# Kernel optimization log

Hardware: AMD Instinct MI355X
Metric: run time of the kernel (lower is better)

## Reference

```python
import jax, jax.numpy as jnp
import numpy as np

B, N, M, D = 4, 2048, 4096, 1
C, K = 4, 32
POINTS_PER_UNIT = 20


def setup_inputs() -> dict:
    key = jax.random.key(0)
    k1, k2, k3 = jax.random.split(key, 3)
    xz = jax.random.uniform(k1, (M, D), dtype=jnp.float32) * 4.0 - 2.0  # grid locations
    x = jax.random.uniform(k2, (B, N, D), dtype=jnp.float32) * 4.0 - 2.0  # target locations
    z = jax.random.normal(k3, (B, C, M, K), dtype=jnp.float32)
    log_scale = jnp.array([np.log(2.0 / POINTS_PER_UNIT)], dtype=jnp.float32)
    return {"xz": xz, "x": x, "z": z, "log_scale": log_scale}


def reference(xz, x, z, log_scale):
    # pairwise squared distances between grid xz [M,D] and targets x [B,N,D] -> [B,M,N]
    d2 = jnp.sum((xz[None, :, None, :] - x[:, None, :, :]) ** 2, axis=-1)
    # RBF weights (note: divided by exp(log_scale), matching original code)
    w = jnp.exp(-0.5 * d2 / jnp.exp(log_scale[0]))  # [B,M,N]
    # weights^T @ z with channel broadcast: [B,C,N,K]
    zt = jnp.einsum('bmn,bcmk->bcnk', w, z)
    # outer product z @ z^T: [B,C,N,N] positive semi-definite
    out = jnp.einsum('bcnk,bcmk->bcnm', zt, zt)
    return (xz, out)
```

## Files before the change

### kernel.cpp

```cpp
#include <hip/hip_runtime.h>
#include <hip/hip_bf16.h>

#define B_   4
#define N_   2048
#define M_   4096
#define C_   4
#define K_   32
#define CK_  128
#define M32_ (M_ / 32)

typedef float f32x4 __attribute__((ext_vector_type(4)));
typedef short s16x8 __attribute__((ext_vector_type(8)));

__device__ __forceinline__ short f2bf(float f) {
    union { __hip_bfloat16 h; short s; } u;
    u.h = __float2bfloat16(f);
    return u.s;
}
__device__ __forceinline__ float bf2f(unsigned short u) {
    return __uint_as_float((unsigned)u << 16);
}

__global__ __launch_bounds__(256) void z2frag_kernel(
    const float* __restrict__ z, unsigned short* __restrict__ zf)
{
    const unsigned u = blockIdx.x * 256 + threadIdx.x;
    const int s   = u & 63;
    const int lg  = s >> 4, l15 = s & 15;
    const int m32 = (u >> 6) & (M32_ - 1);
    const int g   = (u >> 13) & 7;
    const int b   = u >> 16;
    const int c   = g >> 1;
    const int k   = (g & 1) * 16 + l15;
    const int m0  = m32 * 32 + lg * 8;

    const float* src = &z[(((size_t)(b * C_ + c)) * M_ + m0) * K_ + k];
    s16x8 pk;
    #pragma unroll
    for (int e = 0; e < 8; ++e) pk[e] = f2bf(src[(size_t)e * K_]);
    *(s16x8*)&zf[(size_t)u * 8] = pk;
}

template <int MS>
__global__ __launch_bounds__(512, 4) void zt_mfma_kernel(
    const float* __restrict__ xz, const float* __restrict__ x,
    const unsigned short* __restrict__ zf, const float* __restrict__ ls,
    unsigned short* __restrict__ ztp)
{
    constexpr int MCH = M_ / MS;
    constexpr int L   = MCH / 32;
    __shared__ __align__(16) float xz_s[MCH];

    const int tid  = threadIdx.x;
    const int lane = tid & 63;
    const int w    = tid >> 6;
    const int wq   = w >> 1;
    const int wc   = w & 1;
    const int l15  = lane & 15;
    const int lg   = lane >> 4;
    const int ms   = blockIdx.x;
    const int nblk = blockIdx.y * 128;
    const int b    = blockIdx.z;

    const float coef = -0.5f * __expf(-ls[0]);

    float xv[2];
    #pragma unroll
    for (int fa = 0; fa < 2; ++fa)
        xv[fa] = x[b * N_ + nblk + wq * 32 + fa * 16 + l15];

    const int mstart = ms * MCH;
    for (int i = tid; i < MCH; i += 512) xz_s[i] = xz[mstart + i];
    __syncthreads();

    f32x4 acc[2][4];
    #pragma unroll
    for (int i = 0; i < 2; ++i)
        #pragma unroll
        for (int j = 0; j < 4; ++j) acc[i][j] = (f32x4)0.0f;

    const unsigned short* fbase =
        &zf[(((size_t)(b * 8 + wc * 4)) * M32_ + mstart / 32) * 512 + lane * 8];

    s16x8 nb[4];
    #pragma unroll
    for (int fc = 0; fc < 4; ++fc)
        nb[fc] = *(const s16x8*)&fbase[(size_t)fc * M32_ * 512];

    #pragma unroll 4
    for (int ms32 = 0; ms32 < L; ++ms32) {
        s16x8 cb[4];
        #pragma unroll
        for (int fc = 0; fc < 4; ++fc) cb[fc] = nb[fc];
        if (ms32 + 1 < L) {
            #pragma unroll
            for (int fc = 0; fc < 4; ++fc)
                nb[fc] = *(const s16x8*)&fbase[((size_t)fc * M32_ + ms32 + 1) * 512];
        }
        const float* xzp = &xz_s[ms32 * 32 + lg * 8];
        const f32x4 t0 = *reinterpret_cast<const f32x4*>(xzp);
        const f32x4 t1 = *reinterpret_cast<const f32x4*>(xzp + 4);
        const float tt[8] = {t0.x, t0.y, t0.z, t0.w, t1.x, t1.y, t1.z, t1.w};
        s16x8 af[2];
        #pragma unroll
        for (int fa = 0; fa < 2; ++fa) {
            #pragma unroll
            for (int j = 0; j < 8; ++j) {
                const float d = tt[j] - xv[fa];
                af[fa][j] = f2bf(__expf(coef * d * d));
            }
        }
        #pragma unroll
        for (int fa = 0; fa < 2; ++fa)
            #pragma unroll
            for (int fc = 0; fc < 4; ++fc)
                acc[fa][fc] = __builtin_amdgcn_mfma_f32_16x16x32_bf16(
                    af[fa], cb[fc], acc[fa][fc], 0, 0, 0);
    }

    unsigned short* dst = ztp + (size_t)ms * (B_ * C_ * N_ * K_);
    #pragma unroll
    for (int fc = 0; fc < 4; ++fc) {
        const int ck = wc * 64 + fc * 16 + l15;
        const int c  = ck >> 5, k = ck & 31;
        #pragma unroll
        for (int fa = 0; fa < 2; ++fa) {
            const int n0 = nblk + wq * 32 + fa * 16 + lg * 4;
            #pragma unroll
            for (int r = 0; r < 4; ++r)
                dst[(((size_t)b * C_ + c) * N_ + n0 + r) * K_ + k] =
                    (unsigned short)f2bf(acc[fa][fc][r]);
        }
    }
}

template <int MS>
__global__ __launch_bounds__(256) void zt_reduce_copy_kernel(
    const unsigned short* __restrict__ ztp, unsigned short* __restrict__ ztb,
    const float* __restrict__ xz, float* __restrict__ out)
{
    if (blockIdx.x >= 1024) {
        const int t = (blockIdx.x - 1024) * 256 + threadIdx.x;
        *(float4*)&out[t * 4] = *(const float4*)&xz[t * 4];
        return;
    }
    const size_t t      = (size_t)blockIdx.x * 256 + threadIdx.x;
    const size_t stride = (size_t)(B_ * C_ * N_ * K_);
    float s0 = 0.f, s1 = 0.f, s2 = 0.f, s3 = 0.f;
    #pragma unroll
    for (int p = 0; p < MS; ++p) {
        const ushort4 v = *(const ushort4*)&ztp[(size_t)p * stride + t * 4];
        s0 += bf2f(v.x); s1 += bf2f(v.y); s2 += bf2f(v.z); s3 += bf2f(v.w);
    }
    ushort4 pk;
    pk.x = (unsigned short)f2bf(s0); pk.y = (unsigned short)f2bf(s1);
    pk.z = (unsigned short)f2bf(s2); pk.w = (unsigned short)f2bf(s3);
    *(ushort4*)&ztb[t * 4] = pk;
}

#define TB 128
__global__ __launch_bounds__(256, 4) void out_mfma_kernel(
    const unsigned short* __restrict__ ztb, float* __restrict__ out)
{
    __shared__ __align__(16) float t_s[64][132];

    const int tid  = threadIdx.x;
    const int lane = tid & 63;
    const int wave = tid >> 6;
    const int wn   = wave >> 1;
    const int wm   = wave & 1;
    const int l15  = lane & 15;
    const int lg   = lane >> 4;
    const int mblk = blockIdx.x * TB;
    const int nblk = blockIdx.y * TB;
    const int bc   = blockIdx.z;

    const unsigned short* base = ztb + (size_t)bc * (N_ * K_);

    s16x8 afr[4], bfr[4];
    #pragma unroll
    for (int f = 0; f < 4; ++f) {
        const int n = nblk + wn * 64 + f * 16 + l15;
        afr[f] = *reinterpret_cast<const s16x8*>(&base[(size_t)n * K_ + lg * 8]);
        const int m = mblk + wm * 64 + f * 16 + l15;
        bfr[f] = *reinterpret_cast<const s16x8*>(&base[(size_t)m * K_ + lg * 8]);
    }

    f32x4 acc[4][4];
    #pragma unroll
    for (int i = 0; i < 4; ++i)
        #pragma unroll
        for (int j = 0; j < 4; ++j) acc[i][j] = (f32x4)0.0f;

    #pragma unroll
    for (int fa = 0; fa < 4; ++fa)
        #pragma unroll
        for (int fm = 0; fm < 4; ++fm)
            acc[fa][fm] = __builtin_amdgcn_mfma_f32_16x16x32_bf16(
                afr[fa], bfr[fm], acc[fa][fm], 0, 0, 0);

    float* ob = out + (size_t)bc * N_ * N_;

    #pragma unroll
    for (int p = 0; p < 2; ++p) {
        if (p) __syncthreads();
        if (wn == p) {
            #pragma unroll
            for (int fa = 0; fa < 4; ++fa) {
                const int row0 = fa * 16 + lg * 4;
                #pragma unroll
                for (int fm = 0; fm < 4; ++fm) {
                    const int mcol = wm * 64 + fm * 16 + l15;
                    #pragma unroll
                    for (int r = 0; r < 4; ++r)
                        t_s[row0 + r][mcol] = acc[fa][fm][r];
                }
            }
        }
        __syncthreads();
        #pragma unroll
        for (int it = 0; it < 8; ++it) {
            const int e   = tid + it * 256;
            const int row = e >> 5;
            const int c4  = e & 31;
            const f32x4 v = *reinterpret_cast<const f32x4*>(&t_s[row][c4 * 4]);
            *(f32x4*)&ob[(size_t)(nblk + p * 64 + row) * N_ + mblk + c4 * 4] = v;
        }
    }
}

extern "C" void kernel_launch(void* const* d_in, const int* in_sizes, int n_in,
                              void* d_out, int out_size, void* d_ws, size_t ws_size,
                              hipStream_t stream)
{
    const float* xz = (const float*)d_in[0];
    const float* x  = (const float*)d_in[1];
    const float* z  = (const float*)d_in[2];
    const float* ls = (const float*)d_in[3];
    float* out = (float*)d_out;

    (void)in_sizes; (void)n_in; (void)out_size;

    const size_t ztf = (size_t)B_ * C_ * N_ * K_;
    unsigned short* ztb = (unsigned short*)d_ws;
    unsigned short* zf  = ztb + ztf;
    unsigned short* ztp = zf + (size_t)B_ * CK_ * M_;

    z2frag_kernel<<<dim3((unsigned)(B_ * 8 * M32_ * 64 / 256)), dim3(256), 0, stream>>>(z, zf);

    const size_t base_b = ztf * 2 + (size_t)B_ * CK_ * M_ * 2;
    if (ws_size >= base_b + (size_t)8 * ztf * 2) {
        zt_mfma_kernel<8><<<dim3(8, N_ / 128, B_), dim3(512), 0, stream>>>(xz, x, zf, ls, ztp);
        zt_reduce_copy_kernel<8><<<dim3(1028), dim3(256), 0, stream>>>(ztp, ztb, xz, out);
    } else if (ws_size >= base_b + (size_t)4 * ztf * 2) {
        zt_mfma_kernel<4><<<dim3(4, N_ / 128, B_), dim3(512), 0, stream>>>(xz, x, zf, ls, ztp);
        zt_reduce_copy_kernel<4><<<dim3(1028), dim3(256), 0, stream>>>(ztp, ztb, xz, out);
    } else {
        zt_mfma_kernel<2><<<dim3(2, N_ / 128, B_), dim3(512), 0, stream>>>(xz, x, zf, ls, ztp);
        zt_reduce_copy_kernel<2><<<dim3(1028), dim3(256), 0, stream>>>(ztp, ztb, xz, out);
    }

    out_mfma_kernel<<<dim3(N_ / TB, N_ / TB, B_ * C_), dim3(256), 0, stream>>>(ztb, out + M_);
}
```

Measured before the change: 82.56 us.

## Fuse all stages into one persistent kernel with atomic grid barriers

Merges the z fragment conversion, the partial zt MFMA, the split-M reduction and the output outer-product GEMM into a single 512-block persistent kernel. Stages are separated by software grid barriers built on atomic counters, which are reset by a memset before the launch. The aim is to remove the launch overhead and tail gaps of four separate kernels. In exchange the output stage now runs on only 512 blocks looping over 8 tiles each. The barriers also risk deadlock if all 512 blocks are not co-resident, and the larger shared-memory footprint may lower occupancy.

Result: slower. 273.2 us (+230.9%).

```diff
diff --git a/kernel.cpp b/kernel.cpp
--- a/kernel.cpp
+++ b/kernel.cpp
@@ -7,7 +7,10 @@
 #define C_   4
 #define K_   32
 #define CK_  128
-#define M32_ (M_ / 32)
+#define M32_ 128
+#define NBLK 512
+#define THR  512
+#define MS   8
 
 typedef float f32x4 __attribute__((ext_vector_type(4)));
 typedef short s16x8 __attribute__((ext_vector_type(8)));
@@ -21,193 +24,187 @@
     return __uint_as_float((unsigned)u << 16);
 }
 
-__global__ __launch_bounds__(256) void z2frag_kernel(
-    const float* __restrict__ z, unsigned short* __restrict__ zf)
+__device__ __forceinline__ void gridbar(unsigned* c) {
+    __syncthreads();
+    if (threadIdx.x == 0) {
+        __hip_atomic_fetch_add(c, 1u, __ATOMIC_RELEASE, __HIP_MEMORY_SCOPE_AGENT);
+        while (__hip_atomic_load(c, __ATOMIC_ACQUIRE, __HIP_MEMORY_SCOPE_AGENT) < (unsigned)NBLK)
+            __builtin_amdgcn_s_sleep(2);
+    }
+    __syncthreads();
+}
+
+__global__ __launch_bounds__(THR, 4) void fused_kernel(
+    const float* __restrict__ xz, const float* __restrict__ x,
+    const float* __restrict__ z,  const float* __restrict__ ls,
+    float* __restrict__ out, unsigned short* __restrict__ ztb,
+    unsigned short* __restrict__ zf, unsigned short* __restrict__ ztp,
+    unsigned* __restrict__ cnt)
 {
-    const unsigned u = blockIdx.x * 256 + threadIdx.x;
-    const int s   = u & 63;
-    const int lg  = s >> 4, l15 = s & 15;
-    const int m32 = (u >> 6) & (M32_ - 1);
-    const int g   = (u >> 13) & 7;
-    const int b   = u >> 16;
-    const int c   = g >> 1;
-    const int k   = (g & 1) * 16 + l15;
-    const int m0  = m32 * 32 + lg * 8;
-
-    const float* src = &z[(((size_t)(b * C_ + c)) * M_ + m0) * K_ + k];
-    s16x8 pk;
-    #pragma unroll
-    for (int e = 0; e < 8; ++e) pk[e] = f2bf(src[(size_t)e * K_]);
-    *(s16x8*)&zf[(size_t)u * 8] = pk;
-}
-
-template <int MS>
-__global__ __launch_bounds__(512, 4) void zt_mfma_kernel(
-    const float* __restrict__ xz, const float* __restrict__ x,
-    const unsigned short* __restrict__ zf, const float* __restrict__ ls,
-    unsigned short* __restrict__ ztp)
-{
-    constexpr int MCH = M_ / MS;
-    constexpr int L   = MCH / 32;
-    __shared__ __align__(16) float xz_s[MCH];
+    __shared__ __align__(16) float xz_s[M_ / MS];
+    __shared__ __align__(16) float t_s[128][132];
 
     const int tid  = threadIdx.x;
+    const int bid  = blockIdx.x;
+    const int gid  = bid * THR + tid;
     const int lane = tid & 63;
-    const int w    = tid >> 6;
-    const int wq   = w >> 1;
-    const int wc   = w & 1;
     const int l15  = lane & 15;
     const int lg   = lane >> 4;
-    const int ms   = blockIdx.x;
-    const int nblk = blockIdx.y * 128;
-    const int b    = blockIdx.z;
-
-    const float coef = -0.5f * __expf(-ls[0]);
-
-    float xv[2];
-    #pragma unroll
-    for (int fa = 0; fa < 2; ++fa)
-        xv[fa] = x[b * N_ + nblk + wq * 32 + fa * 16 + l15];
-
-    const int mstart = ms * MCH;
-    for (int i = tid; i < MCH; i += 512) xz_s[i] = xz[mstart + i];
-    __syncthreads();
-
-    f32x4 acc[2][4];
-    #pragma unroll
-    for (int i = 0; i < 2; ++i)
-        #pragma unroll
-        for (int j = 0; j < 4; ++j) acc[i][j] = (f32x4)0.0f;
-
-    const unsigned short* fbase =
-        &zf[(((size_t)(b * 8 + wc * 4)) * M32_ + mstart / 32) * 512 + lane * 8];
-
-    s16x8 nb[4];
-    #pragma unroll
-    for (int fc = 0; fc < 4; ++fc)
-        nb[fc] = *(const s16x8*)&fbase[(size_t)fc * M32_ * 512];
-
-    #pragma unroll 4
-    for (int ms32 = 0; ms32 < L; ++ms32) {
-        s16x8 cb[4];
-        #pragma unroll
-        for (int fc = 0; fc < 4; ++fc) cb[fc] = nb[fc];
-        if (ms32 + 1 < L) {
-            #pragma unroll
-            for (int fc = 0; fc < 4; ++fc)
-                nb[fc] = *(const s16x8*)&fbase[((size_t)fc * M32_ + ms32 + 1) * 512];
-        }
-        const float* xzp = &xz_s[ms32 * 32 + lg * 8];
-        const f32x4 t0 = *reinterpret_cast<const f32x4*>(xzp);
-        const f32x4 t1 = *reinterpret_cast<const f32x4*>(xzp + 4);
-        const float tt[8] = {t0.x, t0.y, t0.z, t0.w, t1.x, t1.y, t1.z, t1.w};
-        s16x8 af[2];
-        #pragma unroll
-        for (int fa = 0; fa < 2; ++fa) {
-            #pragma unroll
-            for (int j = 0; j < 8; ++j) {
-                const float d = tt[j] - xv[fa];
-                af[fa][j] = f2bf(__expf(coef * d * d));
-            }
-        }
+    const int w    = tid >> 6;
+
+    {
+        const unsigned u = (unsigned)gid;
+        const int s   = u & 63;
+        const int m32 = (u >> 6) & (M32_ - 1);
+        const int g   = (u >> 13) & 7;
+        const int b   = u >> 16;
+        const int k   = (g & 1) * 16 + (s & 15);
+        const int m0  = m32 * 32 + (s >> 4) * 8;
+        const float* src = &z[(((size_t)(b * C_ + (g >> 1))) * M_ + m0) * K_ + k];
+        s16x8 pk;
+        #pragma unroll
+        for (int e = 0; e < 8; ++e) pk[e] = f2bf(src[(size_t)e * K_]);
+        *(s16x8*)&zf[(size_t)u * 8] = pk;
+        if (gid < 1024) *(f32x4*)&out[gid * 4] = *(const f32x4*)&xz[gid * 4];
+    }
+    gridbar(cnt + 0);
+
+    {
+        constexpr int MCH = M_ / MS;
+        constexpr int L   = MCH / 32;
+        const int ms   = bid & 7;
+        const int nblk = ((bid >> 3) & 15) * 128;
+        const int b    = bid >> 7;
+        const int wq   = w >> 1;
+        const int wc   = w & 1;
+
+        const float coef = -0.5f * __expf(-ls[0]);
+        float xv[2];
         #pragma unroll
         for (int fa = 0; fa < 2; ++fa)
-            #pragma unroll
-            for (int fc = 0; fc < 4; ++fc)
-                acc[fa][fc] = __builtin_amdgcn_mfma_f32_16x16x32_bf16(
-                    af[fa], cb[fc], acc[fa][fc], 0, 0, 0);
-    }
-
-    unsigned short* dst = ztp + (size_t)ms * (B_ * C_ * N_ * K_);
-    #pragma unroll
-    for (int fc = 0; fc < 4; ++fc) {
-        const int ck = wc * 64 + fc * 16 + l15;
-        const int c  = ck >> 5, k = ck & 31;
-        #pragma unroll
-        for (int fa = 0; fa < 2; ++fa) {
-            const int n0 = nblk + wq * 32 + fa * 16 + lg * 4;
-            #pragma unroll
-            for (int r = 0; r < 4; ++r)
-                dst[(((size_t)b * C_ + c) * N_ + n0 + r) * K_ + k] =
-                    (unsigned short)f2bf(acc[fa][fc][r]);
-        }
-    }
-}
-
-template <int MS>
-__global__ __launch_bounds__(256) void zt_reduce_copy_kernel(
-    const unsigned short* __restrict__ ztp, unsigned short* __restrict__ ztb,
-    const float* __restrict__ xz, float* __restrict__ out)
-{
-    if (blockIdx.x >= 1024) {
-        const int t = (blockIdx.x - 1024) * 256 + threadIdx.x;
-        *(float4*)&out[t * 4] = *(const float4*)&xz[t * 4];
-        return;
-    }
-    const size_t t      = (size_t)blockIdx.x * 256 + threadIdx.x;
-    const size_t stride = (size_t)(B_ * C_ * N_ * K_);
-    float s0 = 0.f, s1 = 0.f, s2 = 0.f, s3 = 0.f;
-    #pragma unroll
-    for (int p = 0; p < MS; ++p) {
-        const ushort4 v = *(const ushort4*)&ztp[(size_t)p * stride + t * 4];
-        s0 += bf2f(v.x); s1 += bf2f(v.y); s2 += bf2f(v.z); s3 += bf2f(v.w);
-    }
-    ushort4 pk;
-    pk.x = (unsigned short)f2bf(s0); pk.y = (unsigned short)f2bf(s1);
-    pk.z = (unsigned short)f2bf(s2); pk.w = (unsigned short)f2bf(s3);
-    *(ushort4*)&ztb[t * 4] = pk;
-}
-
-#define TB 128
-__global__ __launch_bounds__(256, 4) void out_mfma_kernel(
-    const unsigned short* __restrict__ ztb, float* __restrict__ out)
-{
-    __shared__ __align__(16) float t_s[64][132];
-
-    const int tid  = threadIdx.x;
-    const int lane = tid & 63;
-    const int wave = tid >> 6;
-    const int wn   = wave >> 1;
-    const int wm   = wave & 1;
-    const int l15  = lane & 15;
-    const int lg   = lane >> 4;
-    const int mblk = blockIdx.x * TB;
-    const int nblk = blockIdx.y * TB;
-    const int bc   = blockIdx.z;
-
-    const unsigned short* base = ztb + (size_t)bc * (N_ * K_);
-
-    s16x8 afr[4], bfr[4];
-    #pragma unroll
-    for (int f = 0; f < 4; ++f) {
-        const int n = nblk + wn * 64 + f * 16 + l15;
-        afr[f] = *reinterpret_cast<const s16x8*>(&base[(size_t)n * K_ + lg * 8]);
-        const int m = mblk + wm * 64 + f * 16 + l15;
-        bfr[f] = *reinterpret_cast<const s16x8*>(&base[(size_t)m * K_ + lg * 8]);
-    }
-
-    f32x4 acc[4][4];
-    #pragma unroll
-    for (int i = 0; i < 4; ++i)
-        #pragma unroll
-        for (int j = 0; j < 4; ++j) acc[i][j] = (f32x4)0.0f;
-
-    #pragma unroll
-    for (int fa = 0; fa < 4; ++fa)
-        #pragma unroll
-        for (int fm = 0; fm < 4; ++fm)
-            acc[fa][fm] = __builtin_amdgcn_mfma_f32_16x16x32_bf16(
-                afr[fa], bfr[fm], acc[fa][fm], 0, 0, 0);
-
-    float* ob = out + (size_t)bc * N_ * N_;
-
-    #pragma unroll
-    for (int p = 0; p < 2; ++p) {
-        if (p) __syncthreads();
-        if (wn == p) {
-            #pragma unroll
-            for (int fa = 0; fa < 4; ++fa) {
-                const int row0 = fa * 16 + lg * 4;
+            xv[fa] = x[b * N_ + nblk + wq * 32 + fa * 16 + l15];
+
+        const int mstart = ms * MCH;
+        xz_s[tid] = xz[mstart + tid];
+        __syncthreads();
+
+        f32x4 acc[2][4];
+        #pragma unroll
+        for (int i = 0; i < 2; ++i)
+            #pragma unroll
+            for (int j = 0; j < 4; ++j) acc[i][j] = (f32x4)0.0f;
+
+        const unsigned short* fbase =
+            &zf[(((size_t)(b * 8 + wc * 4)) * M32_ + mstart / 32) * 512 + lane * 8];
+
+        s16x8 nb[4];
+        #pragma unroll
+        for (int fc = 0; fc < 4; ++fc)
+            nb[fc] = *(const s16x8*)&fbase[(size_t)fc * M32_ * 512];
+
+        #pragma unroll 4
+        for (int ms32 = 0; ms32 < L; ++ms32) {
+            s16x8 cb[4];
+            #pragma unroll
+            for (int fc = 0; fc < 4; ++fc) cb[fc] = nb[fc];
+            if (ms32 + 1 < L) {
+                #pragma unroll
+                for (int fc = 0; fc < 4; ++fc)
+                    nb[fc] = *(const s16x8*)&fbase[((size_t)fc * M32_ + ms32 + 1) * 512];
+            }
+            const float* xzp = &xz_s[ms32 * 32 + lg * 8];
+            const f32x4 t0 = *reinterpret_cast<const f32x4*>(xzp);
+            const f32x4 t1 = *reinterpret_cast<const f32x4*>(xzp + 4);
+            const float tt[8] = {t0.x, t0.y, t0.z, t0.w, t1.x, t1.y, t1.z, t1.w};
+            s16x8 af[2];
+            #pragma unroll
+            for (int fa = 0; fa < 2; ++fa) {
+                #pragma unroll
+                for (int j = 0; j < 8; ++j) {
+                    const float d = tt[j] - xv[fa];
+                    af[fa][j] = f2bf(__expf(coef * d * d));
+                }
+            }
+            #pragma unroll
+            for (int fa = 0; fa < 2; ++fa)
+                #pragma unroll
+                for (int fc = 0; fc < 4; ++fc)
+                    acc[fa][fc] = __builtin_amdgcn_mfma_f32_16x16x32_bf16(
+                        af[fa], cb[fc], acc[fa][fc], 0, 0, 0);
+        }
+
+        unsigned short* dst = ztp + (size_t)ms * (B_ * C_ * N_ * K_);
+        #pragma unroll
+        for (int fc = 0; fc < 4; ++fc) {
+            const int ck = wc * 64 + fc * 16 + l15;
+            const int c  = ck >> 5, k = ck & 31;
+            #pragma unroll
+            for (int fa = 0; fa < 2; ++fa) {
+                const int n0 = nblk + wq * 32 + fa * 16 + lg * 4;
+                #pragma unroll
+                for (int r = 0; r < 4; ++r)
+                    dst[(((size_t)b * C_ + c) * N_ + n0 + r) * K_ + k] =
+                        (unsigned short)f2bf(acc[fa][fc][r]);
+            }
+        }
+    }
+    gridbar(cnt + 1);
+
+    {
+        const size_t t      = (size_t)gid;
+        const size_t stride = (size_t)(B_ * C_ * N_ * K_);
+        float s0 = 0.f, s1 = 0.f, s2 = 0.f, s3 = 0.f;
+        #pragma unroll
+        for (int p = 0; p < MS; ++p) {
+            const ushort4 v = *(const ushort4*)&ztp[(size_t)p * stride + t * 4];
+            s0 += bf2f(v.x); s1 += bf2f(v.y); s2 += bf2f(v.z); s3 += bf2f(v.w);
+        }
+        ushort4 pk;
+        pk.x = (unsigned short)f2bf(s0); pk.y = (unsigned short)f2bf(s1);
+        pk.z = (unsigned short)f2bf(s2); pk.w = (unsigned short)f2bf(s3);
+        *(ushort4*)&ztb[t * 4] = pk;
+    }
+    gridbar(cnt + 2);
+
+    {
+        const int wn = w >> 1;
+        const int wm = w & 1;
+        for (int i = 0; i < 8; ++i) {
+            const int tile = bid * 8 + i;
+            const int mblk = (tile & 15) * 128;
+            const int nblk = ((tile >> 4) & 15) * 128;
+            const int bc   = tile >> 8;
+            const unsigned short* base = ztb + (size_t)bc * (N_ * K_);
+
+            s16x8 afr[2], bfr[4];
+            #pragma unroll
+            for (int fa = 0; fa < 2; ++fa) {
+                const int n = nblk + wn * 32 + fa * 16 + l15;
+                afr[fa] = *reinterpret_cast<const s16x8*>(&base[(size_t)n * K_ + lg * 8]);
+            }
+            #pragma unroll
+            for (int fm = 0; fm < 4; ++fm) {
+                const int m = mblk + wm * 64 + fm * 16 + l15;
+                bfr[fm] = *reinterpret_cast<const s16x8*>(&base[(size_t)m * K_ + lg * 8]);
+            }
+
+            f32x4 acc[2][4];
+            #pragma unroll
+            for (int a = 0; a < 2; ++a)
+                #pragma unroll
+                for (int b2 = 0; b2 < 4; ++b2) acc[a][b2] = (f32x4)0.0f;
+
+            #pragma unroll
+            for (int fa = 0; fa < 2; ++fa)
+                #pragma unroll
+                for (int fm = 0; fm < 4; ++fm)
+                    acc[fa][fm] = __builtin_amdgcn_mfma_f32_16x16x32_bf16(
+                        afr[fa], bfr[fm], acc[fa][fm], 0, 0, 0);
+
+            __syncthreads();
+            #pragma unroll
+            for (int fa = 0; fa < 2; ++fa) {
+                const int row0 = wn * 32 + fa * 16 + lg * 4;
                 #pragma unroll
                 for (int fm = 0; fm < 4; ++fm) {
                     const int mcol = wm * 64 + fm * 16 + l15;
@@ -216,15 +213,17 @@
                         t_s[row0 + r][mcol] = acc[fa][fm][r];
                 }
             }
-        }
-        __syncthreads();
-        #pragma unroll
-        for (int it = 0; it < 8; ++it) {
-            const int e   = tid + it * 256;
-            const int row = e >> 5;
-            const int c4  = e & 31;
-            const f32x4 v = *reinterpret_cast<const f32x4*>(&t_s[row][c4 * 4]);
-            *(f32x4*)&ob[(size_t)(nblk + p * 64 + row) * N_ + mblk + c4 * 4] = v;
+            __syncthreads();
+
+            float* ob = out + M_ + (size_t)bc * N_ * N_;
+            #pragma unroll
+            for (int it = 0; it < 8; ++it) {
+                const int e   = tid + it * THR;
+                const int row = e >> 5;
+                const int c4  = e & 31;
+                const f32x4 v = *reinterpret_cast<const f32x4*>(&t_s[row][c4 * 4]);
+                *(f32x4*)&ob[(size_t)(nblk + row) * N_ + mblk + c4 * 4] = v;
+            }
         }
     }
 }
@@ -239,26 +238,13 @@
     const float* ls = (const float*)d_in[3];
     float* out = (float*)d_out;
 
-    (void)in_sizes; (void)n_in; (void)out_size;
-
-    const size_t ztf = (size_t)B_ * C_ * N_ * K_;
-    unsigned short* ztb = (unsigned short*)d_ws;
-    unsigned short* zf  = ztb + ztf;
+    (void)in_sizes; (void)n_in; (void)out_size; (void)ws_size;
+
+    unsigned* cnt       = (unsigned*)d_ws;
+    unsigned short* ztb = (unsigned short*)((char*)d_ws + 16);
+    unsigned short* zf  = ztb + (size_t)B_ * C_ * N_ * K_;
     unsigned short* ztp = zf + (size_t)B_ * CK_ * M_;
 
-    z2frag_kernel<<<dim3((unsigned)(B_ * 8 * M32_ * 64 / 256)), dim3(256), 0, stream>>>(z, zf);
-
-    const size_t base_b = ztf * 2 + (size_t)B_ * CK_ * M_ * 2;
-    if (ws_size >= base_b + (size_t)8 * ztf * 2) {
-        zt_mfma_kernel<8><<<dim3(8, N_ / 128, B_), dim3(512), 0, stream>>>(xz, x, zf, ls, ztp);
-        zt_reduce_copy_kernel<8><<<dim3(1028), dim3(256), 0, stream>>>(ztp, ztb, xz, out);
-    } else if (ws_size >= base_b + (size_t)4 * ztf * 2) {
-        zt_mfma_kernel<4><<<dim3(4, N_ / 128, B_), dim3(512), 0, stream>>>(xz, x, zf, ls, ztp);
-        zt_reduce_copy_kernel<4><<<dim3(1028), dim3(256), 0, stream>>>(ztp, ztb, xz, out);
-    } else {
-        zt_mfma_kernel<2><<<dim3(2, N_ / 128, B_), dim3(512), 0, stream>>>(xz, x, zf, ls, ztp);
-        zt_reduce_copy_kernel<2><<<dim3(1028), dim3(256), 0, stream>>>(ztp, ztb, xz, out);
-    }
-
-    out_mfma_kernel<<<dim3(N_ / TB, N_ / TB, B_ * C_), dim3(256), 0, stream>>>(ztb, out + M_);
-}
+    hipMemsetAsync(cnt, 0, 16, stream);
+    fused_kernel<<<dim3(NBLK), dim3(THR), 0, stream>>>(xz, x, z, ls, out, ztb, zf, ztp, cnt);
+}
```

## Exploit symmetry of Gram output: compute upper-triangular tiles and mirror-store transpose

Applied to the files above, without the earlier changes.

The output kernel now launches only the upper-triangular 128x128 tiles, 136 per batch-channel, recovering tile indices from a triangular-number decode. Each off-diagonal tile also writes its transpose, staged through a second LDS buffer, to the mirrored location. This roughly halves the MFMA work and the fragment loads, while the output store traffic, which dominates this write-bound stage, stays the same. It costs more shared memory, lower occupancy (launch bounds 4 to 2), and strided transposed LDS writes.

Measured after the change: 79.26 us. 1.04x faster.

```diff
diff --git a/kernel.cpp b/kernel.cpp
--- a/kernel.cpp
+++ b/kernel.cpp
@@ -7,7 +7,7 @@
 #define C_   4
 #define K_   32
 #define CK_  128
-#define M32_ (M_ / 32)
+#define M32_ 128
 
 typedef float f32x4 __attribute__((ext_vector_type(4)));
 typedef short s16x8 __attribute__((ext_vector_type(8)));
@@ -158,11 +158,11 @@
     *(ushort4*)&ztb[t * 4] = pk;
 }
 
-#define TB 128
-__global__ __launch_bounds__(256, 4) void out_mfma_kernel(
+__global__ __launch_bounds__(256, 2) void out_mfma_sym_kernel(
     const unsigned short* __restrict__ ztb, float* __restrict__ out)
 {
     __shared__ __align__(16) float t_s[64][132];
+    __shared__ __align__(16) float t2 [128][68];
 
     const int tid  = threadIdx.x;
     const int lane = tid & 63;
@@ -171,9 +171,15 @@
     const int wm   = wave & 1;
     const int l15  = lane & 15;
     const int lg   = lane >> 4;
-    const int mblk = blockIdx.x * TB;
-    const int nblk = blockIdx.y * TB;
-    const int bc   = blockIdx.z;
+
+    const int xid = blockIdx.x;
+    int tj = (int)((sqrtf(8.f * xid + 1.f) - 1.f) * 0.5f);
+    while (tj * (tj + 1) / 2 > xid) --tj;
+    while ((tj + 1) * (tj + 2) / 2 <= xid) ++tj;
+    const int ti   = xid - tj * (tj + 1) / 2;
+    const int nblk = ti * 128;
+    const int mblk = tj * 128;
+    const int bc   = blockIdx.y;
 
     const unsigned short* base = ztb + (size_t)bc * (N_ * K_);
 
@@ -200,6 +206,7 @@
                 afr[fa], bfr[fm], acc[fa][fm], 0, 0, 0);
 
     float* ob = out + (size_t)bc * N_ * N_;
+    const bool offdiag = (ti != tj);
 
     #pragma unroll
     for (int p = 0; p < 2; ++p) {
@@ -214,6 +221,7 @@
                     #pragma unroll
                     for (int r = 0; r < 4; ++r)
                         t_s[row0 + r][mcol] = acc[fa][fm][r];
+                    *(f32x4*)&t2[mcol][row0] = acc[fa][fm];
                 }
             }
         }
@@ -225,6 +233,16 @@
             const int c4  = e & 31;
             const f32x4 v = *reinterpret_cast<const f32x4*>(&t_s[row][c4 * 4]);
             *(f32x4*)&ob[(size_t)(nblk + p * 64 + row) * N_ + mblk + c4 * 4] = v;
+        }
+        if (offdiag) {
+            #pragma unroll
+            for (int it = 0; it < 8; ++it) {
+                const int e    = tid + it * 256;
+                const int mrow = e >> 4;
+                const int nc4  = e & 15;
+                const f32x4 v  = *reinterpret_cast<const f32x4*>(&t2[mrow][nc4 * 4]);
+                *(f32x4*)&ob[(size_t)(mblk + mrow) * N_ + nblk + p * 64 + nc4 * 4] = v;
+            }
         }
     }
 }
@@ -260,5 +278,5 @@
         zt_reduce_copy_kernel<2><<<dim3(1028), dim3(256), 0, stream>>>(ztp, ztb, xz, out);
     }
 
-    out_mfma_kernel<<<dim3(N_ / TB, N_ / TB, B_ * C_), dim3(256), 0, stream>>>(ztb, out + M_);
-}
+    out_mfma_sym_kernel<<<dim3(136, B_ * C_), dim3(256), 0, stream>>>(ztb, out + M_);
+}
```
